# Optimization experiments

Measured on AMD Instinct MI355X. Metric: run time of the kernel, lower is better.

## Reference

```python
import jax, jax.numpy as jnp
import numpy as np


def _sage(x_src, x_dst, src, dst, Wl, bl, Wr, num_dst):
    # PyG SAGEConv with mean aggregation: lin_l(mean_{j->i} x_src[j]) + lin_r(x_dst[i])
    msg = x_src[src]                                   # [E, d] gather
    agg = jax.ops.segment_sum(msg, dst, num_segments=num_dst)          # [Nd, d]
    cnt = jax.ops.segment_sum(jnp.ones_like(dst, dtype=x_src.dtype), dst,
                              num_segments=num_dst)                     # [Nd]
    mean = agg / jnp.maximum(cnt, 1.0)[:, None]
    return mean @ Wl + bl + x_dst @ Wr                 # [Nd, d_out]


def setup_inputs() -> dict:
    key = jax.random.key(0)
    ks = jax.random.split(key, 16)
    Na, Nb, E, D = 200000, 100000, 500000, 128
    s = 1.0 / np.sqrt(D)
    inp = {
        'x_a': jax.random.normal(ks[0], (Na, D), jnp.float32),
        'x_b': jax.random.normal(ks[1], (Nb, D), jnp.float32),
        'e0_src': jax.random.randint(ks[2], (E,), 0, Na, jnp.int32),
        'e0_dst': jax.random.randint(ks[3], (E,), 0, Na, jnp.int32),
        'e1_src': jax.random.randint(ks[4], (E,), 0, Na, jnp.int32),
        'e1_dst': jax.random.randint(ks[5], (E,), 0, Nb, jnp.int32),
        'e2_src': jax.random.randint(ks[6], (E,), 0, Nb, jnp.int32),
        'e2_dst': jax.random.randint(ks[7], (E,), 0, Na, jnp.int32),
        'Wl0': jax.random.normal(ks[8], (D, D), jnp.float32) * s,
        'bl0': jnp.zeros((D,), jnp.float32),
        'Wr0': jax.random.normal(ks[9], (D, D), jnp.float32) * s,
        'Wl1': jax.random.normal(ks[10], (D, D), jnp.float32) * s,
        'bl1': jnp.zeros((D,), jnp.float32),
        'Wr1': jax.random.normal(ks[11], (D, D), jnp.float32) * s,
        'Wl2': jax.random.normal(ks[12], (D, D), jnp.float32) * s,
        'bl2': jnp.zeros((D,), jnp.float32),
        'Wr2': jax.random.normal(ks[13], (D, D), jnp.float32) * s,
        'rel_logits': jnp.zeros((3,), jnp.float32),
    }
    return inp


def reference(x_a, x_b, e0_src, e0_dst, e1_src, e1_dst, e2_src, e2_dst,
              Wl0, bl0, Wr0, Wl1, bl1, Wr1, Wl2, bl2, Wr2, rel_logits):
    Na, Nb = x_a.shape[0], x_b.shape[0]
    rw = jax.nn.softmax(rel_logits)
    # relation 0: a -> a (self node type), 1: a -> b, 2: b -> a
    h0 = _sage(x_a, x_a, e0_src, e0_dst, Wl0, bl0, Wr0, Na)
    h1 = _sage(x_a, x_b, e1_src, e1_dst, Wl1, bl1, Wr1, Nb)
    h2 = _sage(x_b, x_a, e2_src, e2_dst, Wl2, bl2, Wr2, Na)
    out_a = rw[0] * h0 + rw[2] * h2
    out_b = rw[1] * h1
    return out_a, out_b, rw
```

## Files before the change

kernel.cpp:

```cpp
#include <hip/hip_runtime.h>
#include <hip/hip_bf16.h>

#define DD 128
#define CAP02 16
#define CAP1 32
#define OVFC 4096

typedef float f32x4 __attribute__((ext_vector_type(4)));
typedef __bf16 bf16x8 __attribute__((ext_vector_type(8)));

__global__ void prep_kernel(const float* __restrict__ Wl0, const float* __restrict__ bl0, const float* __restrict__ Wr0,
                            const float* __restrict__ Wl1, const float* __restrict__ bl1, const float* __restrict__ Wr1,
                            const float* __restrict__ Wl2, const float* __restrict__ bl2, const float* __restrict__ Wr2,
                            const float* __restrict__ rl,
                            __bf16* __restrict__ WtA, __bf16* __restrict__ Wtb,
                            float* __restrict__ ba, float* __restrict__ bb,
                            float* __restrict__ rw_out) {
    const int n = threadIdx.x;
    float l0 = rl[0], l1 = rl[1], l2 = rl[2];
    float mx = fmaxf(l0, fmaxf(l1, l2));
    float e0 = expf(l0 - mx), e1 = expf(l1 - mx), e2 = expf(l2 - mx);
    float s = e0 + e1 + e2;
    float r0 = e0 / s, r1 = e1 / s, r2 = e2 / s;
    for (int k = 0; k < DD; k++) {
        WtA[n * 384 + k]       = (__bf16)(r0 * Wl0[k * DD + n]);
        WtA[n * 384 + 128 + k] = (__bf16)(r0 * Wr0[k * DD + n] + r2 * Wr2[k * DD + n]);
        WtA[n * 384 + 256 + k] = (__bf16)(r2 * Wl2[k * DD + n]);
        Wtb[n * 256 + k]       = (__bf16)(r1 * Wl1[k * DD + n]);
        Wtb[n * 256 + 128 + k] = (__bf16)(r1 * Wr1[k * DD + n]);
    }
    ba[n] = r0 * bl0[n] + r2 * bl2[n];
    bb[n] = r1 * bl1[n];
    if (n < 3) rw_out[n] = (n == 0 ? r0 : (n == 1 ? r1 : r2));
}

__global__ __launch_bounds__(256) void fill_bucket(const int* __restrict__ src, const int* __restrict__ dst,
                                                   int E, int Nd, int Ns, int cap,
                                                   int* __restrict__ cnt, int* __restrict__ bucket,
                                                   int* __restrict__ ovf_cnt, int2* __restrict__ ovf) {
    int e = blockIdx.x * 256 + threadIdx.x;
    if (e >= E) return;
    int d = dst[e];
    if (d < 0 || d >= Nd) return;
    int s = src[e];
    if (s < 0 || s >= Ns) return;
    int slot = atomicAdd(&cnt[d], 1);
    if (slot < cap) bucket[(size_t)d * cap + slot] = s;
    else { int o = atomicAdd(ovf_cnt, 1); if (o < OVFC) ovf[o] = make_int2(d, s); }
}

template <int KSRC>
__global__ __launch_bounds__(64) void fused_tile(const float* __restrict__ XA,
                                                 const float* __restrict__ XB,
                                                 const float* __restrict__ XR,
                                                 const int* __restrict__ C0, const int* __restrict__ BK0, int cap0,
                                                 const int* __restrict__ C2, const int* __restrict__ BK2, int cap2,
                                                 const __bf16* __restrict__ Wt,
                                                 const float* __restrict__ bias,
                                                 float* __restrict__ out, int Nrows) {
    constexpr int K = KSRC * 128;
    constexpr int KP = 136;
    __shared__ __bf16 A[16 * KP];
    const int lane = threadIdx.x;
    const int t = blockIdx.x;
    const int c2 = lane * 2;
    const int m = lane & 15, g = lane >> 4;

    f32x4 acc[8];
#pragma unroll
    for (int n = 0; n < 8; n++) acc[n] = (f32x4)0.0f;

#pragma unroll
    for (int sec = 0; sec < KSRC; sec++) {
        if (sec == 1) {
#pragma unroll
            for (int r = 0; r < 16; r++) {
                const int row = t * 16 + r;
                float2 v = make_float2(0.f, 0.f);
                if (row < Nrows) v = ((const float2*)(XR + (size_t)row * DD))[lane];
                A[r * KP + c2] = (__bf16)v.x;
                A[r * KP + c2 + 1] = (__bf16)v.y;
            }
        } else {
            const int* cnt = (sec == 0) ? C0 : C2;
            const int* bkp = (sec == 0) ? BK0 : BK2;
            const int cap  = (sec == 0) ? cap0 : cap2;
            const float* X = (sec == 0) ? XA : XB;
            int du[16];
            float ax[16], ay[16];
            int mdu = 0;
#pragma unroll
            for (int r = 0; r < 16; r++) {
                const int row = t * 16 + r;
                int d = (row < Nrows) ? cnt[row] : 0;
                du[r] = d < cap ? d : cap;
                if (du[r] > mdu) mdu = du[r];
                ax[r] = 0.f; ay[r] = 0.f;
            }
            for (int i = 0; i < mdu; i++) {
#pragma unroll
                for (int r = 0; r < 16; r++) {
                    if (i < du[r]) {
                        const int s = bkp[(size_t)(t * 16 + r) * cap + i];
                        const float2 v = ((const float2*)(X + (size_t)s * DD))[lane];
                        ax[r] += v.x; ay[r] += v.y;
                    }
                }
            }
#pragma unroll
            for (int r = 0; r < 16; r++) {
                const int row = t * 16 + r;
                const float sc = (row < Nrows) ? 1.0f / fmaxf((float)cnt[row], 1.0f) : 0.f;
                A[r * KP + c2] = (__bf16)(ax[r] * sc);
                A[r * KP + c2 + 1] = (__bf16)(ay[r] * sc);
            }
        }
        __syncthreads();
#pragma unroll
        for (int ks = 0; ks < 4; ks++) {
            const int koff = ks * 32 + g * 8;
            const bf16x8 a = *(const bf16x8*)(&A[m * KP + koff]);
#pragma unroll
            for (int n = 0; n < 8; n++) {
                const bf16x8 b = *(const bf16x8*)(Wt + (size_t)(n * 16 + m) * K + sec * 128 + koff);
                acc[n] = __builtin_amdgcn_mfma_f32_16x16x32_bf16(a, b, acc[n], 0, 0, 0);
            }
        }
        __syncthreads();
    }

#pragma unroll
    for (int n = 0; n < 8; n++) {
        const int col = n * 16 + m;
        const float bv = bias[col];
#pragma unroll
        for (int r = 0; r < 4; r++) {
            const int orow = t * 16 + g * 4 + r;
            if (orow < Nrows) out[(size_t)orow * DD + col] = acc[n][r] + bv;
        }
    }
}

__global__ __launch_bounds__(128) void ovf_fix(const int* __restrict__ ovfc, const int2* __restrict__ ovf,
                                               const float* __restrict__ x, const int* __restrict__ cnt,
                                               const __bf16* __restrict__ Wt, int K, int sec,
                                               float* __restrict__ out) {
    int m = *ovfc;
    if (m > OVFC) m = OVFC;
    const int n = threadIdx.x;
    for (int i = blockIdx.x; i < m; i += gridDim.x) {
        const int2 p = ovf[i];
        const float sc = 1.0f / fmaxf((float)cnt[p.x], 1.0f);
        float acc = 0.f;
        for (int k = 0; k < DD; k++)
            acc += x[(size_t)p.y * DD + k] * (float)Wt[(size_t)n * K + sec + k];
        atomicAdd(&out[(size_t)p.x * DD + n], acc * sc);
    }
}

extern "C" void kernel_launch(void* const* d_in, const int* in_sizes, int n_in,
                              void* d_out, int out_size, void* d_ws, size_t ws_size,
                              hipStream_t stream) {
    if (n_in != 18) return;

    const float* x_a = (const float*)d_in[0];
    const float* x_b = (const float*)d_in[1];
    const int* e0_src = (const int*)d_in[2];
    const int* e0_dst = (const int*)d_in[3];
    const int* e1_src = (const int*)d_in[4];
    const int* e1_dst = (const int*)d_in[5];
    const int* e2_src = (const int*)d_in[6];
    const int* e2_dst = (const int*)d_in[7];
    const float* Wl0 = (const float*)d_in[8];
    const float* bl0 = (const float*)d_in[9];
    const float* Wr0 = (const float*)d_in[10];
    const float* Wl1 = (const float*)d_in[11];
    const float* bl1 = (const float*)d_in[12];
    const float* Wr1 = (const float*)d_in[13];
    const float* Wl2 = (const float*)d_in[14];
    const float* bl2 = (const float*)d_in[15];
    const float* Wr2 = (const float*)d_in[16];
    const float* rl  = (const float*)d_in[17];

    const int Na = in_sizes[0] / DD;
    const int Nb = in_sizes[1] / DD;
    const int E0 = in_sizes[2], E1 = in_sizes[4], E2 = in_sizes[6];

    float* out_f = (float*)d_out;
    float* out_a = out_f;
    float* out_b = out_f + (size_t)Na * DD;
    float* rw_out = out_f + (size_t)Na * DD + (size_t)Nb * DD;

    char* base = (char*)d_ws;
    size_t off = 0;
    auto alloc = [&](size_t bytes) { char* r = base + off; off += (bytes + 511) & ~(size_t)511; return r; };
    int* cnt0 = (int*)alloc((size_t)Na * 4);
    int* cnt1 = (int*)alloc((size_t)Nb * 4);
    int* cnt2 = (int*)alloc((size_t)Na * 4);
    int* ovfc = (int*)alloc(512);
    int2* ovf0 = (int2*)alloc(OVFC * 8);
    int2* ovf1 = (int2*)alloc(OVFC * 8);
    int2* ovf2 = (int2*)alloc(OVFC * 8);
    size_t zero_hi = off;
    __bf16* WtA = (__bf16*)alloc(128 * 384 * 2);
    __bf16* Wtb = (__bf16*)alloc(128 * 256 * 2);
    float* ba = (float*)alloc(512);
    float* bb = (float*)alloc(512);
    size_t b0cap = (size_t)Na * CAP02;
    size_t b1cap = (size_t)Nb * CAP1;
    int* bucket0 = (int*)alloc((b0cap > b1cap ? b0cap : b1cap) * 4);
    int* bucket2 = (int*)alloc((size_t)Na * CAP02 * 4);
    int* bucket1 = bucket0;
    if (ws_size < off) return;

    hipMemsetAsync(d_ws, 0, zero_hi, stream);
    prep_kernel<<<1, 128, 0, stream>>>(Wl0, bl0, Wr0, Wl1, bl1, Wr1, Wl2, bl2, Wr2, rl,
                                       WtA, Wtb, ba, bb, rw_out);

    const int fb0 = (E0 + 255) / 256, fb1 = (E1 + 255) / 256, fb2 = (E2 + 255) / 256;

    fill_bucket<<<fb1, 256, 0, stream>>>(e1_src, e1_dst, E1, Nb, Na, CAP1, cnt1, bucket1, ovfc + 1, ovf1);
    fused_tile<2><<<(Nb + 15) / 16, 64, 0, stream>>>(x_a, nullptr, x_b,
                                                     cnt1, bucket1, CAP1,
                                                     nullptr, nullptr, 0,
                                                     Wtb, bb, out_b, Nb);
    ovf_fix<<<32, 128, 0, stream>>>(ovfc + 1, ovf1, x_a, cnt1, Wtb, 256, 0, out_b);

    fill_bucket<<<fb0, 256, 0, stream>>>(e0_src, e0_dst, E0, Na, Na, CAP02, cnt0, bucket0, ovfc + 0, ovf0);
    fill_bucket<<<fb2, 256, 0, stream>>>(e2_src, e2_dst, E2, Na, Nb, CAP02, cnt2, bucket2, ovfc + 2, ovf2);
    fused_tile<3><<<(Na + 15) / 16, 64, 0, stream>>>(x_a, x_b, x_a,
                                                     cnt0, bucket0, CAP02,
                                                     cnt2, bucket2, CAP02,
                                                     WtA, ba, out_a, Na);
    ovf_fix<<<32, 128, 0, stream>>>(ovfc + 0, ovf0, x_a, cnt0, WtA, 384, 0, out_a);
    ovf_fix<<<32, 128, 0, stream>>>(ovfc + 2, ovf2, x_b, cnt2, WtA, 384, 256, out_a);
}
```

Measured before the change: 573.1 us.

## Interleave both mean-aggregation gathers and load root features directly into MFMA operands

The fused tile kernel now computes both neighbor-mean aggregations (relations 0 and 2) before any MFMA work and keeps them in two separate shared-memory tiles, so their gather loops run back to back without intervening barriers. The root-feature section is loaded straight from global memory into MFMA A operands as float4 pairs converted to bf16, which skips staging it through LDS. Per-section syncthreads are removed and a launch-bounds occupancy hint of 3 blocks is added. Together these aim to cut barrier stalls and LDS traffic. The cost is more registers and LDS per block, plus uncoalesced row-wise global reads for the root tile.

Result: faster. 561.0 us (-2.1%).

```diff
diff --git a/kernel.cpp b/kernel.cpp
--- a/kernel.cpp
+++ b/kernel.cpp
@@ -50,83 +50,114 @@
 }
 
 template <int KSRC>
-__global__ __launch_bounds__(64) void fused_tile(const float* __restrict__ XA,
-                                                 const float* __restrict__ XB,
-                                                 const float* __restrict__ XR,
-                                                 const int* __restrict__ C0, const int* __restrict__ BK0, int cap0,
-                                                 const int* __restrict__ C2, const int* __restrict__ BK2, int cap2,
-                                                 const __bf16* __restrict__ Wt,
-                                                 const float* __restrict__ bias,
-                                                 float* __restrict__ out, int Nrows) {
+__global__ __launch_bounds__(64, 3) void fused_tile(const float* __restrict__ XA,
+                                                    const float* __restrict__ XB,
+                                                    const float* __restrict__ XR,
+                                                    const int* __restrict__ C0, const int* __restrict__ BK0, int cap0,
+                                                    const int* __restrict__ C2, const int* __restrict__ BK2, int cap2,
+                                                    const __bf16* __restrict__ Wt,
+                                                    const float* __restrict__ bias,
+                                                    float* __restrict__ out, int Nrows) {
     constexpr int K = KSRC * 128;
+    constexpr int NMEAN = KSRC - 1;
     constexpr int KP = 136;
-    __shared__ __bf16 A[16 * KP];
+    __shared__ __bf16 A[NMEAN][16 * KP];
     const int lane = threadIdx.x;
     const int t = blockIdx.x;
     const int c2 = lane * 2;
     const int m = lane & 15, g = lane >> 4;
 
-    f32x4 acc[8];
-#pragma unroll
-    for (int n = 0; n < 8; n++) acc[n] = (f32x4)0.0f;
-
-#pragma unroll
-    for (int sec = 0; sec < KSRC; sec++) {
-        if (sec == 1) {
+    {
+        int du0[16];
+        float a0x[16], a0y[16];
+        int mdu0 = 0;
+#pragma unroll
+        for (int r = 0; r < 16; r++) {
+            const int row = t * 16 + r;
+            int d = (row < Nrows) ? C0[row] : 0;
+            du0[r] = d < cap0 ? d : cap0;
+            if (du0[r] > mdu0) mdu0 = du0[r];
+            a0x[r] = 0.f; a0y[r] = 0.f;
+        }
+        int du2[16];
+        float a2x[16], a2y[16];
+        int mdu2 = 0;
+        if (NMEAN == 2) {
 #pragma unroll
             for (int r = 0; r < 16; r++) {
                 const int row = t * 16 + r;
-                float2 v = make_float2(0.f, 0.f);
-                if (row < Nrows) v = ((const float2*)(XR + (size_t)row * DD))[lane];
-                A[r * KP + c2] = (__bf16)v.x;
-                A[r * KP + c2 + 1] = (__bf16)v.y;
-            }
-        } else {
-            const int* cnt = (sec == 0) ? C0 : C2;
-            const int* bkp = (sec == 0) ? BK0 : BK2;
-            const int cap  = (sec == 0) ? cap0 : cap2;
-            const float* X = (sec == 0) ? XA : XB;
-            int du[16];
-            float ax[16], ay[16];
-            int mdu = 0;
+                int d = (row < Nrows) ? C2[row] : 0;
+                du2[r] = d < cap2 ? d : cap2;
+                if (du2[r] > mdu2) mdu2 = du2[r];
+                a2x[r] = 0.f; a2y[r] = 0.f;
+            }
+        }
+        for (int i = 0; i < mdu0; i++) {
 #pragma unroll
             for (int r = 0; r < 16; r++) {
-                const int row = t * 16 + r;
-                int d = (row < Nrows) ? cnt[row] : 0;
-                du[r] = d < cap ? d : cap;
-                if (du[r] > mdu) mdu = du[r];
-                ax[r] = 0.f; ay[r] = 0.f;
-            }
-            for (int i = 0; i < mdu; i++) {
+                if (i < du0[r]) {
+                    const int s = BK0[(size_t)(t * 16 + r) * cap0 + i];
+                    const float2 v = ((const float2*)(XA + (size_t)s * DD))[lane];
+                    a0x[r] += v.x; a0y[r] += v.y;
+                }
+            }
+        }
+        if (NMEAN == 2) {
+            for (int i = 0; i < mdu2; i++) {
 #pragma unroll
                 for (int r = 0; r < 16; r++) {
-                    if (i < du[r]) {
-                        const int s = bkp[(size_t)(t * 16 + r) * cap + i];
-                        const float2 v = ((const float2*)(X + (size_t)s * DD))[lane];
-                        ax[r] += v.x; ay[r] += v.y;
+                    if (i < du2[r]) {
+                        const int s = BK2[(size_t)(t * 16 + r) * cap2 + i];
+                        const float2 v = ((const float2*)(XB + (size_t)s * DD))[lane];
+                        a2x[r] += v.x; a2y[r] += v.y;
                     }
                 }
             }
-#pragma unroll
-            for (int r = 0; r < 16; r++) {
-                const int row = t * 16 + r;
-                const float sc = (row < Nrows) ? 1.0f / fmaxf((float)cnt[row], 1.0f) : 0.f;
-                A[r * KP + c2] = (__bf16)(ax[r] * sc);
-                A[r * KP + c2 + 1] = (__bf16)(ay[r] * sc);
-            }
-        }
-        __syncthreads();
+        }
+#pragma unroll
+        for (int r = 0; r < 16; r++) {
+            const int row = t * 16 + r;
+            const float sc0 = (row < Nrows) ? 1.0f / fmaxf((float)C0[row], 1.0f) : 0.f;
+            A[0][r * KP + c2] = (__bf16)(a0x[r] * sc0);
+            A[0][r * KP + c2 + 1] = (__bf16)(a0y[r] * sc0);
+            if (NMEAN == 2) {
+                const float sc2 = (row < Nrows) ? 1.0f / fmaxf((float)C2[row], 1.0f) : 0.f;
+                A[1][r * KP + c2] = (__bf16)(a2x[r] * sc2);
+                A[1][r * KP + c2 + 1] = (__bf16)(a2y[r] * sc2);
+            }
+        }
+    }
+    __syncthreads();
+
+    const int xrow = t * 16 + m;
+    const float* xp = XR + (size_t)(xrow < Nrows ? xrow : 0) * DD;
+    f32x4 acc[8];
+#pragma unroll
+    for (int n = 0; n < 8; n++) acc[n] = (f32x4)0.0f;
+
+#pragma unroll
+    for (int sec = 0; sec < KSRC; sec++) {
 #pragma unroll
         for (int ks = 0; ks < 4; ks++) {
             const int koff = ks * 32 + g * 8;
-            const bf16x8 a = *(const bf16x8*)(&A[m * KP + koff]);
+            bf16x8 a;
+            if (sec == 1) {
+                const float4 v0 = ((const float4*)(xp + koff))[0];
+                const float4 v1 = ((const float4*)(xp + koff))[1];
+                a[0] = (__bf16)v0.x; a[1] = (__bf16)v0.y;
+                a[2] = (__bf16)v0.z; a[3] = (__bf16)v0.w;
+                a[4] = (__bf16)v1.x; a[5] = (__bf16)v1.y;
+                a[6] = (__bf16)v1.z; a[7] = (__bf16)v1.w;
+            } else {
+                const int mi = (sec == 0) ? 0 : 1;
+                a = *(const bf16x8*)(&A[mi][m * KP + koff]);
+            }
 #pragma unroll
             for (int n = 0; n < 8; n++) {
                 const bf16x8 b = *(const bf16x8*)(Wt + (size_t)(n * 16 + m) * K + sec * 128 + koff);
                 acc[n] = __builtin_amdgcn_mfma_f32_16x16x32_bf16(a, b, acc[n], 0, 0, 0);
             }
         }
-        __syncthreads();
     }
 
 #pragma unroll
```
